# Optimization experiments

Measured on AMD Instinct MI355X. Metric: run time of the kernel, lower is better.

The kernel has to match this reference:

```python
import jax, jax.numpy as jnp
import numpy as np

DIM = 512
D_IN = 4096
N_OBJ = 2048
N_REL = 32768
STEPS = 2
N_OBJ_CLS = 151
N_REL_CLS = 51
EPS = 1e-5


def _mlp2(x, w1, b1, w2, b2):
    # Linear -> ReLU -> Linear (torch Linear: y = x W^T + b)
    return jnp.maximum(x @ w1.T + b1, 0.0) @ w2.T + b2


def _gate(a, b, w, bias):
    # Sequential(Linear(2*dim, 1), Sigmoid) on cat([a, b], 1)
    return jax.nn.sigmoid(jnp.concatenate([a, b], axis=1) @ w.T + bias)


def _gru_cell(x, h, wih, whh, bih, bhh):
    gi = x @ wih.T + bih  # [N, 3*DIM]
    gh = h @ whh.T + bhh
    ir, iz, inew = jnp.split(gi, 3, axis=1)
    hr, hz, hnew = jnp.split(gh, 3, axis=1)
    r = jax.nn.sigmoid(ir + hr)
    z = jax.nn.sigmoid(iz + hz)
    n = jnp.tanh(inew + r * hnew)
    return (1.0 - z) * n + z * h


def setup_inputs() -> dict:
    key = jax.random.key(0)
    ks = jax.random.split(key, 32)
    rn = lambda k, shape, s=0.02: jax.random.normal(k, shape, dtype=jnp.float32) * s
    z = lambda *shape: jnp.zeros(shape, dtype=jnp.float32)
    return {
        'x_obj': jax.random.normal(ks[0], (N_OBJ, D_IN), dtype=jnp.float32),
        'x_pred': jax.random.normal(ks[1], (N_REL, D_IN), dtype=jnp.float32),
        'rel_inds': jax.random.randint(ks[2], (N_REL, 2), 0, N_OBJ),
        # obj / pred embedding MLPs
        'oe_w1': rn(ks[3], (DIM, D_IN)), 'oe_b1': z(DIM),
        'oe_w2': rn(ks[4], (DIM, DIM)), 'oe_b2': z(DIM),
        'pe_w1': rn(ks[5], (DIM, D_IN)), 'pe_b1': z(DIM),
        'pe_w2': rn(ks[6], (DIM, DIM)), 'pe_b2': z(DIM),
        # gates: Linear(2*dim, 1)
        'g_sn_w': rn(ks[7], (1, 2 * DIM)), 'g_sn_b': z(1),
        'g_on_w': rn(ks[8], (1, 2 * DIM)), 'g_on_b': z(1),
        'g_se_w': rn(ks[9], (1, 2 * DIM)), 'g_se_b': z(1),
        'g_oe_w': rn(ks[10], (1, 2 * DIM)), 'g_oe_b': z(1),
        # GRU cells
        'ngru_wih': rn(ks[11], (3 * DIM, DIM)), 'ngru_whh': rn(ks[12], (3 * DIM, DIM)),
        'ngru_bih': z(3 * DIM), 'ngru_bhh': z(3 * DIM),
        'egru_wih': rn(ks[13], (3 * DIM, DIM)), 'egru_whh': rn(ks[14], (3 * DIM, DIM)),
        'egru_bih': z(3 * DIM), 'egru_bhh': z(3 * DIM),
        # classifier heads
        'op_w': rn(ks[15], (N_OBJ_CLS, DIM)), 'op_b': z(N_OBJ_CLS),
        'pp_w': rn(ks[16], (N_REL_CLS, DIM)), 'pp_b': z(N_REL_CLS),
    }


def reference(x_obj, x_pred, rel_inds,
              oe_w1, oe_b1, oe_w2, oe_b2,
              pe_w1, pe_b1, pe_w2, pe_b2,
              g_sn_w, g_sn_b, g_on_w, g_on_b,
              g_se_w, g_se_b, g_oe_w, g_oe_b,
              ngru_wih, ngru_whh, ngru_bih, ngru_bhh,
              egru_wih, egru_whh, egru_bih, egru_bhh,
              op_w, op_b, pp_w, pp_b):
    n_obj = x_obj.shape[0]
    subj_idx = rel_inds[:, 0]
    obj_idx = rel_inds[:, 1]

    h_obj = _mlp2(x_obj, oe_w1, oe_b1, oe_w2, oe_b2)    # [N_obj, DIM]
    h_edge = _mlp2(x_pred, pe_w1, pe_b1, pe_w2, pe_b2)  # [N_rel, DIM]

    # row sums of the 0/1 subj/obj_pred_map == in-degree counts (constants)
    ones = jnp.ones((rel_inds.shape[0],), dtype=jnp.float32)
    cnt_s = jax.ops.segment_sum(ones, subj_idx, num_segments=n_obj)[:, None]
    cnt_o = jax.ops.segment_sum(ones, obj_idx, num_segments=n_obj)[:, None]

    for _ in range(STEPS):
        sub_vert = h_obj[subj_idx]  # [N_rel, DIM]
        obj_vert = h_obj[obj_idx]

        # node update: gated edge->node messages, mean-aggregated per node
        msg_p2s = _gate(sub_vert, h_edge, g_sn_w, g_sn_b) * h_edge
        msg_p2o = _gate(obj_vert, h_edge, g_on_w, g_on_b) * h_edge
        node_message = (
            jax.ops.segment_sum(msg_p2s, subj_idx, num_segments=n_obj) / (cnt_s + EPS)
            + jax.ops.segment_sum(msg_p2o, obj_idx, num_segments=n_obj) / (cnt_o + EPS)
        ) / 2.0
        new_h_obj = _gru_cell(node_message, h_obj, ngru_wih, ngru_whh, ngru_bih, ngru_bhh)

        # edge update: gated node->edge messages
        msg_s2p = _gate(sub_vert, h_edge, g_se_w, g_se_b) * sub_vert
        msg_o2p = _gate(obj_vert, h_edge, g_oe_w, g_oe_b) * obj_vert
        edge_message = (msg_s2p + msg_o2p) / 2.0
        h_edge = _gru_cell(edge_message, h_edge, egru_wih, egru_whh, egru_bih, egru_bhh)
        h_obj = new_h_obj

    obj_class_logits = h_obj @ op_w.T + op_b    # [N_obj, 151]
    pred_class_logits = h_edge @ pp_w.T + pp_b  # [N_rel, 51]
    obj_class_labels = jnp.argmax(obj_class_logits[:, 1:], axis=1) + 1
    return (h_obj, h_edge, obj_class_logits, pred_class_logits, obj_class_labels, rel_inds)
```

## Files before the change

kernel.cpp:

```cpp
#include <hip/hip_runtime.h>
#include <math.h>

typedef unsigned short u16;
typedef unsigned int u32;
typedef _Float16 f16;
typedef f16 f16x8 __attribute__((ext_vector_type(8)));
typedef float f32x4 __attribute__((ext_vector_type(4)));

#define DIM 512
#define D_IN 4096
#define N_OBJS 2048
#define N_RELS 32768
#define N_OBJ_CLS 151
#define N_REL_CLS 51
#define EPSV 1e-5f

#define OFF_HOBJ  0
#define OFF_HEDGE (N_OBJS*DIM)
#define OFF_OLOG  (OFF_HEDGE + N_RELS*DIM)
#define OFF_PLOG  (OFF_OLOG + N_OBJS*N_OBJ_CLS)
#define OFF_LBL   (OFF_PLOG + N_RELS*N_REL_CLS)
#define OFF_RI    (OFF_LBL + N_OBJS)

__device__ __forceinline__ float sigmoidf_(float x) { return 1.0f / (1.0f + expf(-x)); }
__device__ __forceinline__ u16 f2h_(float f) {
    union { f16 h; u16 u; } c; c.h = (f16)f; return c.u;
}
__device__ __forceinline__ float h2f_(u16 u) {
    union { f16 h; u16 u; } c; c.u = u; return (float)c.h;
}

__device__ __forceinline__ void cvt8h1(const float* f, uint4& h) {
    u32 hh[8];
#pragma unroll
    for (int i = 0; i < 8; i++) hh[i] = f2h_(f[i]);
    h.x = hh[0] | (hh[1] << 16); h.y = hh[2] | (hh[3] << 16);
    h.z = hh[4] | (hh[5] << 16); h.w = hh[6] | (hh[7] << 16);
}
__device__ __forceinline__ void cvt8h2(const float* f, uint4& h, uint4& l) {
    u32 hh[8], ll[8];
#pragma unroll
    for (int i = 0; i < 8; i++) {
        u16 x = f2h_(f[i]);
        hh[i] = x;
        ll[i] = f2h_(f[i] - h2f_(x));
    }
    h.x = hh[0] | (hh[1] << 16); h.y = hh[2] | (hh[3] << 16);
    h.z = hh[4] | (hh[5] << 16); h.w = hh[6] | (hh[7] << 16);
    l.x = ll[0] | (ll[1] << 16); l.y = ll[2] | (ll[3] << 16);
    l.z = ll[4] | (ll[5] << 16); l.w = ll[6] | (ll[7] << 16);
}

__device__ __forceinline__ int swzo(int row, int c) {
    return row * 32 + ((c ^ ((row >> 1) & 3)) << 3);
}

__device__ __forceinline__ int xcdswz(int orig, int nwg) {
    const int q = nwg >> 3;
    return (orig & 7) * q + (orig >> 3);
}

__device__ __forceinline__ void gload16(const void* g, void* l) {
    __builtin_amdgcn_global_load_lds(
        (const __attribute__((address_space(1))) void*)g,
        (__attribute__((address_space(3))) void*)l, 16, 0, 0);
}

#define Q_BIG  (DIM * D_IN / 4)
#define Q_SQ   (DIM * DIM / 4)
#define Q_GRU  (3 * DIM * DIM / 4)
#define Q_OP   (N_OBJ_CLS * DIM / 4)
#define Q_PP   (N_REL_CLS * DIM / 4)
#define CV_C0  (Q_BIG)
#define CV_C1  (CV_C0 + Q_BIG)
#define CV_C2  (CV_C1 + Q_SQ)
#define CV_C3  (CV_C2 + Q_SQ)
#define CV_C4  (CV_C3 + Q_GRU)
#define CV_C5  (CV_C4 + Q_GRU)
#define CV_C6  (CV_C5 + Q_GRU)
#define CV_C7  (CV_C6 + Q_GRU)
#define CV_C8  (CV_C7 + Q_OP)
#define CV_C9  (CV_C8 + Q_PP)

__global__ __launch_bounds__(256) void convert_all(
    const float* __restrict__ s0, u16* __restrict__ d0,
    const float* __restrict__ s1, u16* __restrict__ d1,
    const float* __restrict__ s2, u16* __restrict__ d2,
    const float* __restrict__ s3, u16* __restrict__ d3,
    const float* __restrict__ s4, u16* __restrict__ d4,
    const float* __restrict__ s5, u16* __restrict__ d5,
    const float* __restrict__ s6, u16* __restrict__ d6,
    const float* __restrict__ s7, u16* __restrict__ d7,
    const float* __restrict__ s8, u16* __restrict__ d8,
    const float* __restrict__ s9, u16* __restrict__ d9)
{
    int i = blockIdx.x * 256 + threadIdx.x;
    if (i >= CV_C9) return;
    const float* src; u16* dst; int base;
    if      (i < CV_C0) { src = s0; dst = d0; base = 0; }
    else if (i < CV_C1) { src = s1; dst = d1; base = CV_C0; }
    else if (i < CV_C2) { src = s2; dst = d2; base = CV_C1; }
    else if (i < CV_C3) { src = s3; dst = d3; base = CV_C2; }
    else if (i < CV_C4) { src = s4; dst = d4; base = CV_C3; }
    else if (i < CV_C5) { src = s5; dst = d5; base = CV_C4; }
    else if (i < CV_C6) { src = s6; dst = d6; base = CV_C5; }
    else if (i < CV_C7) { src = s7; dst = d7; base = CV_C6; }
    else if (i < CV_C8) { src = s8; dst = d8; base = CV_C7; }
    else                { src = s9; dst = d9; base = CV_C8; }
    const int q = i - base;
    const float4 v = ((const float4*)src)[q];
    ((ushort4*)dst)[q] = make_ushort4(f2h_(v.x), f2h_(v.y), f2h_(v.z), f2h_(v.w));
}

template<bool RELU, int AT, bool WSPLIT>
__device__ __forceinline__ void gemm_a32_body(
    int id, u16* sAh, u16* sBh, u16* sAl,
    const float* __restrict__ A, const u16* __restrict__ Bhi,
    const float* __restrict__ bias, u16* __restrict__ Chi, u16* __restrict__ Clo,
    int NX, int K)
{
    const int m0 = (id / NX) * 128, n0 = (id % NX) * 128;
    const int N = NX * 128;
    const int t = threadIdx.x;
    const int wid = t >> 6, lane = t & 63;
    const int wm = (wid >> 1) * 64, wn = (wid & 1) * 64;
    const int lr = lane & 15, lk = lane >> 4;

    f32x4 acc[4][4] = {};

    const int sr = t >> 1;
    const int sc = (t & 1) * 2;
    const float* Ap = A + (size_t)(m0 + sr) * K + (t & 1) * 16;

    const int rB = (wid * 2) * 16 + (lane >> 2);
    const int cB = (lane & 3) ^ ((rB >> 1) & 3);
    const u16* Bp0 = Bhi + (size_t)(n0 + rB) * K + cB * 8;
    const u16* Bp1 = Bp0 + (size_t)16 * K;
    u16* Bd0 = &sBh[(wid * 2) * 512];
    u16* Bd1 = Bd0 + 512;

    float fv[16];
    *(float4*)&fv[0]  = *(const float4*)(Ap);
    *(float4*)&fv[4]  = *(const float4*)(Ap + 4);
    *(float4*)&fv[8]  = *(const float4*)(Ap + 8);
    *(float4*)&fv[12] = *(const float4*)(Ap + 12);

    for (int k0 = 0; k0 < K; k0 += 32) {
        uint4 ah0, ah1, al0, al1;
        if (AT == 2) { cvt8h2(fv, ah0, al0); cvt8h2(fv + 8, ah1, al1); }
        else         { cvt8h1(fv, ah0);      cvt8h1(fv + 8, ah1); }

        __syncthreads();
        gload16(Bp0 + k0, Bd0);
        gload16(Bp1 + k0, Bd1);
        *(uint4*)&sAh[swzo(sr, sc)]     = ah0;
        *(uint4*)&sAh[swzo(sr, sc + 1)] = ah1;
        if (AT == 2) {
            *(uint4*)&sAl[swzo(sr, sc)]     = al0;
            *(uint4*)&sAl[swzo(sr, sc + 1)] = al1;
        }
        asm volatile("s_waitcnt vmcnt(0)" ::: "memory");
        __syncthreads();

        const int kn = k0 + 32;
        if (kn < K) {
            *(float4*)&fv[0]  = *(const float4*)(Ap + kn);
            *(float4*)&fv[4]  = *(const float4*)(Ap + kn + 4);
            *(float4*)&fv[8]  = *(const float4*)(Ap + kn + 8);
            *(float4*)&fv[12] = *(const float4*)(Ap + kn + 12);
        }

        f16x8 ah[4], al[4], bh[4];
#pragma unroll
        for (int f = 0; f < 4; f++) {
            const int off = swzo(wm + f * 16 + lr, lk);
            ah[f] = *(const f16x8*)&sAh[off];
            if (AT == 2) al[f] = *(const f16x8*)&sAl[off];
            bh[f] = *(const f16x8*)&sBh[swzo(wn + f * 16 + lr, lk)];
        }
#pragma unroll
        for (int fm = 0; fm < 4; fm++)
#pragma unroll
            for (int fn = 0; fn < 4; fn++) {
                acc[fm][fn] = __builtin_amdgcn_mfma_f32_16x16x32_f16(ah[fm], bh[fn], acc[fm][fn], 0, 0, 0);
                if (AT == 2)
                    acc[fm][fn] = __builtin_amdgcn_mfma_f32_16x16x32_f16(al[fm], bh[fn], acc[fm][fn], 0, 0, 0);
            }
    }
#pragma unroll
    for (int fm = 0; fm < 4; fm++) {
        const int mrow = m0 + wm + fm * 16 + lk * 4;
#pragma unroll
        for (int fn = 0; fn < 4; fn++) {
            const int col = n0 + wn + fn * 16 + lr;
            const float bv = bias[col];
#pragma unroll
            for (int j = 0; j < 4; j++) {
                float v = acc[fm][fn][j] + bv;
                if (RELU) v = fmaxf(v, 0.0f);
                const u16 h = f2h_(v);
                Chi[(size_t)(mrow + j) * N + col] = h;
                if (WSPLIT) Clo[(size_t)(mrow + j) * N + col] = f2h_(v - h2f_(h));
            }
        }
    }
}

__global__ __launch_bounds__(256, 3) void enc1_both(
    const float* __restrict__ xp, const u16* __restrict__ pw,
    const float* __restrict__ pb, u16* __restrict__ tmpe,
    const float* __restrict__ xo, const u16* __restrict__ ow,
    const float* __restrict__ ob, u16* __restrict__ tmpoh, u16* __restrict__ tmpol)
{
    __shared__ u16 smem[3 * 4096];
    const int id = xcdswz(blockIdx.x, gridDim.x);
    if (id < 1024)
        gemm_a32_body<true, 1, false>(id, smem, smem + 4096, nullptr,
                                      xp, pw, pb, tmpe, nullptr, 4, D_IN);
    else
        gemm_a32_body<true, 2, true>(id - 1024, smem, smem + 4096, smem + 8192,
                                     xo, ow, ob, tmpoh, tmpol, 4, D_IN);
}

template<int AT, bool WF32, bool WHI, bool WLO>
__device__ __forceinline__ void gemm_f16_body(
    int id, u16* smem,
    const u16* __restrict__ Ahi, const u16* __restrict__ Alo,
    const u16* __restrict__ Bhi, const float* __restrict__ bias,
    float* __restrict__ C32, u16* __restrict__ Chi, u16* __restrict__ Clo,
    int NX, int N, int ldc, int K)
{
    const int m0 = (id / NX) * 128, n0 = (id % NX) * 128;
    const int t = threadIdx.x;
    const int wid = t >> 6, lane = t & 63;
    const int wm = (wid >> 1) * 64, wn = (wid & 1) * 64;
    const int lr = lane & 15, lk = lane >> 4;

    f32x4 acc[4][4] = {};

    const int rr = (wid * 2) * 16 + (lane >> 2);
    const int cc = (lane & 3) ^ ((rr >> 1) & 3);
    const u16* pA0 = Ahi + (size_t)(m0 + rr) * K + cc * 8;
    const u16* pA1 = pA0 + (size_t)16 * K;
    const u16* pL0 = (AT == 2) ? Alo + (size_t)(m0 + rr) * K + cc * 8 : nullptr;
    const u16* pL1 = (AT == 2) ? pL0 + (size_t)16 * K : nullptr;
    const u16* pB0 = Bhi + (size_t)(n0 + rr) * K + cc * 8;
    const u16* pB1 = pB0 + (size_t)16 * K;
    const int bOff = (wid * 2) * 512;

    for (int k0 = 0; k0 < K; k0 += 64) {
        __syncthreads();
#pragma unroll
        for (int h = 0; h < 2; h++) {
            const int kk = k0 + h * 32;
            u16* sA_ = smem + h * 4096;
            u16* sB_ = smem + 8192 + h * 4096;
            gload16(pA0 + kk, sA_ + bOff);
            gload16(pA1 + kk, sA_ + bOff + 512);
            if (AT == 2) {
                u16* sL_ = smem + 16384 + h * 4096;
                gload16(pL0 + kk, sL_ + bOff);
                gload16(pL1 + kk, sL_ + bOff + 512);
            }
            gload16(pB0 + kk, sB_ + bOff);
            gload16(pB1 + kk, sB_ + bOff + 512);
        }
        asm volatile("s_waitcnt vmcnt(0)" ::: "memory");
        __syncthreads();

#pragma unroll
        for (int h = 0; h < 2; h++) {
            const u16* sA_ = smem + h * 4096;
            const u16* sB_ = smem + 8192 + h * 4096;
            const u16* sL_ = smem + 16384 + h * 4096;
            f16x8 ah[4], al[4], bh[4];
#pragma unroll
            for (int f = 0; f < 4; f++) {
                const int off = swzo(wm + f * 16 + lr, lk);
                ah[f] = *(const f16x8*)&sA_[off];
                if (AT == 2) al[f] = *(const f16x8*)&sL_[off];
                bh[f] = *(const f16x8*)&sB_[swzo(wn + f * 16 + lr, lk)];
            }
#pragma unroll
            for (int fm = 0; fm < 4; fm++)
#pragma unroll
                for (int fn = 0; fn < 4; fn++) {
                    acc[fm][fn] = __builtin_amdgcn_mfma_f32_16x16x32_f16(ah[fm], bh[fn], acc[fm][fn], 0, 0, 0);
                    if (AT == 2)
                        acc[fm][fn] = __builtin_amdgcn_mfma_f32_16x16x32_f16(al[fm], bh[fn], acc[fm][fn], 0, 0, 0);
                }
        }
    }
#pragma unroll
    for (int fm = 0; fm < 4; fm++) {
        const int mrow = m0 + wm + fm * 16 + lk * 4;
#pragma unroll
        for (int fn = 0; fn < 4; fn++) {
            const int col = n0 + wn + fn * 16 + lr;
            const float bv = bias[col];
#pragma unroll
            for (int j = 0; j < 4; j++) {
                const float v = acc[fm][fn][j] + bv;
                if (WF32 && col < N) C32[(size_t)(mrow + j) * ldc + col] = v;
                if (WHI) {
                    const u16 h = f2h_(v);
                    Chi[(size_t)(mrow + j) * (NX * 128) + col] = h;
                    if (WLO)
                        Clo[(size_t)(mrow + j) * (NX * 128) + col] = f2h_(v - h2f_(h));
                }
            }
        }
    }
}

template<int AT, bool WF32, bool WHI, bool WLO>
__global__ __launch_bounds__(256, AT == 1 ? 4 : 3) void gemm_f16(
    const u16* __restrict__ Ahi, const u16* __restrict__ Alo,
    const u16* __restrict__ Bhi, const float* __restrict__ bias,
    float* __restrict__ C32, u16* __restrict__ Chi, u16* __restrict__ Clo,
    int NX, int N, int ldc, int K)
{
    __shared__ u16 smem[AT == 2 ? 6 * 4096 : 4 * 4096];
    const int id = xcdswz(blockIdx.x, gridDim.x);
    gemm_f16_body<AT, WF32, WHI, WLO>(id, smem, Ahi, Alo, Bhi, bias,
                                      C32, Chi, Clo, NX, N, ldc, K);
}

__global__ __launch_bounds__(256, 3) void cls_both(
    const u16* __restrict__ hhe, const u16* __restrict__ pph,
    const float* __restrict__ ppb, float* __restrict__ plog,
    const u16* __restrict__ hhoh, const u16* __restrict__ hhol,
    const u16* __restrict__ oph, const float* __restrict__ opb,
    float* __restrict__ olog)
{
    __shared__ u16 smem[6 * 4096];
    const int id = xcdswz(blockIdx.x, gridDim.x);
    if (id < 256)
        gemm_f16_body<1, true, false, false>(id, smem, hhe, nullptr, pph, ppb,
                                             plog, nullptr, nullptr,
                                             1, N_REL_CLS, N_REL_CLS, DIM);
    else
        gemm_f16_body<2, true, false, false>(id - 256, smem, hhoh, hhol, oph, opb,
                                             olog, nullptr, nullptr,
                                             2, N_OBJ_CLS, N_OBJ_CLS, DIM);
}

__global__ __launch_bounds__(256, 4) void gru_gemm_e(
    const u16* __restrict__ Xh, const u16* __restrict__ WiH,
    const float* __restrict__ bi, u16* __restrict__ gi,
    const u16* __restrict__ Hh, const u16* __restrict__ WhH,
    const float* __restrict__ bhs, u16* __restrict__ gh_)
{
    __shared__ u16 smem[4 * 4096];
    const int id = xcdswz(blockIdx.x, gridDim.x);
    const int part = id % 24;
    const int m0b = id / 24;
    const bool isH = part >= 12;
    const int nblk = part - (isH ? 12 : 0);
    gemm_f16_body<1, false, true, false>(m0b * 12 + nblk, smem,
        isH ? Hh : Xh, nullptr, isH ? WhH : WiH, isH ? bhs : bi,
        nullptr, isH ? gh_ : gi, nullptr, 12, 1536, 1536, DIM);
}

__global__ __launch_bounds__(256, 4) void gru_all1(
    const u16* __restrict__ Xe, const u16* __restrict__ WeI,
    const float* __restrict__ beI, u16* __restrict__ geI,
    const u16* __restrict__ He, const u16* __restrict__ WeH,
    const float* __restrict__ beH, u16* __restrict__ geH,
    int nEdge,
    const u16* __restrict__ Xoh, const u16* __restrict__ Xol,
    const u16* __restrict__ Hoh, const u16* __restrict__ Hol,
    const u16* __restrict__ WoI, const u16* __restrict__ WoH,
    const float* __restrict__ boI, const float* __restrict__ boH,
    const float* __restrict__ zb,
    u16* __restrict__ gioh, u16* __restrict__ giol,
    u16* __restrict__ ghoh, u16* __restrict__ ghol)
{
    __shared__ u16 smem[4 * 4096];
    const int id = xcdswz(blockIdx.x, gridDim.x);
    if (id < nEdge) {
        const int part = id % 24;
        const int m0b = id / 24;
        const bool isH = part >= 12;
        const int nblk = part - (isH ? 12 : 0);
        gemm_f16_body<1, false, true, false>(m0b * 12 + nblk, smem,
            isH ? He : Xe, nullptr, isH ? WeH : WeI, isH ? beH : beI,
            nullptr, isH ? geH : geI, nullptr, 12, 1536, 1536, DIM);
    } else if (id < nEdge + 384) {
        const int oid = id - nEdge;
        const int part = oid % 24;
        const int m0b = oid / 24;
        const bool isH = part >= 12;
        const int nblk = part - (isH ? 12 : 0);
        gemm_f16_body<1, false, true, false>(m0b * 12 + nblk, smem,
            isH ? Hoh : Xoh, nullptr, isH ? WoH : WoI, isH ? boH : boI,
            nullptr, isH ? ghoh : gioh, nullptr, 12, 1536, 1536, DIM);
    } else {
        const int oid = id - nEdge - 384;
        const int part = oid % 24;
        const int m0b = oid / 24;
        const bool isH = part >= 12;
        const int nblk = part - (isH ? 12 : 0);
        gemm_f16_body<1, false, true, false>(m0b * 12 + nblk, smem,
            isH ? Hol : Xol, nullptr, isH ? WoH : WoI, zb,
            nullptr, isH ? ghol : giol, nullptr, 12, 1536, 1536, DIM);
    }
}

__device__ __forceinline__ float gcomb(float ir, float iz, float in_,
                                       float hr, float hz, float hn, float h) {
    const float r = sigmoidf_(ir + hr);
    const float z = sigmoidf_(iz + hz);
    const float n = tanhf(in_ + r * hn);
    return (1.0f - z) * n + z * h;
}

template<bool WF32>
__global__ __launch_bounds__(256) void gru_combine(
    const u16* __restrict__ gi, const u16* __restrict__ gh,
    u16* __restrict__ hh, float* __restrict__ H32, int R)
{
    const int idx = blockIdx.x * 256 + threadIdx.x;
    if (idx >= R * 128) return;
    const int r = idx >> 7, c4 = (idx & 127) * 4;
    const size_t gb = (size_t)r * 1536 + c4;
    const ushort4 ir4 = *(const ushort4*)&gi[gb];
    const ushort4 iz4 = *(const ushort4*)&gi[gb + 512];
    const ushort4 in4 = *(const ushort4*)&gi[gb + 1024];
    const ushort4 hr4 = *(const ushort4*)&gh[gb];
    const ushort4 hz4 = *(const ushort4*)&gh[gb + 512];
    const ushort4 hn4 = *(const ushort4*)&gh[gb + 1024];
    const size_t hb = (size_t)r * 512 + c4;
    const ushort4 hhi = *(const ushort4*)&hh[hb];
    float4 o;
    o.x = gcomb(h2f_(ir4.x), h2f_(iz4.x), h2f_(in4.x),
                h2f_(hr4.x), h2f_(hz4.x), h2f_(hn4.x), h2f_(hhi.x));
    o.y = gcomb(h2f_(ir4.y), h2f_(iz4.y), h2f_(in4.y),
                h2f_(hr4.y), h2f_(hz4.y), h2f_(hn4.y), h2f_(hhi.y));
    o.z = gcomb(h2f_(ir4.z), h2f_(iz4.z), h2f_(in4.z),
                h2f_(hr4.z), h2f_(hz4.z), h2f_(hn4.z), h2f_(hhi.z));
    o.w = gcomb(h2f_(ir4.w), h2f_(iz4.w), h2f_(in4.w),
                h2f_(hr4.w), h2f_(hz4.w), h2f_(hn4.w), h2f_(hhi.w));
    *(ushort4*)&hh[hb] = make_ushort4(f2h_(o.x), f2h_(o.y), f2h_(o.z), f2h_(o.w));
    if (WF32) *(float4*)&H32[hb] = o;
}

template<bool WF32>
__global__ __launch_bounds__(256) void gru_combine_o2(
    const u16* __restrict__ gih, const u16* __restrict__ gil,
    const u16* __restrict__ ghh_, const u16* __restrict__ ghl_,
    u16* __restrict__ hh, u16* __restrict__ hl, float* __restrict__ H32, int R)
{
    const int idx = blockIdx.x * 256 + threadIdx.x;
    if (idx >= R * 128) return;
    const int r = idx >> 7, c4 = (idx & 127) * 4;
    const size_t gb = (size_t)r * 1536 + c4;
    ushort4 a, b;
    float ir[4], iz[4], in_[4], hr[4], hz[4], hn[4];
    a = *(const ushort4*)&gih[gb];        b = *(const ushort4*)&gil[gb];
    ir[0] = h2f_(a.x) + h2f_(b.x); ir[1] = h2f_(a.y) + h2f_(b.y);
    ir[2] = h2f_(a.z) + h2f_(b.z); ir[3] = h2f_(a.w) + h2f_(b.w);
    a = *(const ushort4*)&gih[gb + 512];  b = *(const ushort4*)&gil[gb + 512];
    iz[0] = h2f_(a.x) + h2f_(b.x); iz[1] = h2f_(a.y) + h2f_(b.y);
    iz[2] = h2f_(a.z) + h2f_(b.z); iz[3] = h2f_(a.w) + h2f_(b.w);
    a = *(const ushort4*)&gih[gb + 1024]; b = *(const ushort4*)&gil[gb + 1024];
    in_[0] = h2f_(a.x) + h2f_(b.x); in_[1] = h2f_(a.y) + h2f_(b.y);
    in_[2] = h2f_(a.z) + h2f_(b.z); in_[3] = h2f_(a.w) + h2f_(b.w);
    a = *(const ushort4*)&ghh_[gb];        b = *(const ushort4*)&ghl_[gb];
    hr[0] = h2f_(a.x) + h2f_(b.x); hr[1] = h2f_(a.y) + h2f_(b.y);
    hr[2] = h2f_(a.z) + h2f_(b.z); hr[3] = h2f_(a.w) + h2f_(b.w);
    a = *(const ushort4*)&ghh_[gb + 512];  b = *(const ushort4*)&ghl_[gb + 512];
    hz[0] = h2f_(a.x) + h2f_(b.x); hz[1] = h2f_(a.y) + h2f_(b.y);
    hz[2] = h2f_(a.z) + h2f_(b.z); hz[3] = h2f_(a.w) + h2f_(b.w);
    a = *(const ushort4*)&ghh_[gb + 1024]; b = *(const ushort4*)&ghl_[gb + 1024];
    hn[0] = h2f_(a.x) + h2f_(b.x); hn[1] = h2f_(a.y) + h2f_(b.y);
    hn[2] = h2f_(a.z) + h2f_(b.z); hn[3] = h2f_(a.w) + h2f_(b.w);

    const size_t hb = (size_t)r * 512 + c4;
    const ushort4 hhi = *(const ushort4*)&hh[hb];
    const ushort4 hlo = *(const ushort4*)&hl[hb];
    float h[4];
    h[0] = h2f_(hhi.x) + h2f_(hlo.x); h[1] = h2f_(hhi.y) + h2f_(hlo.y);
    h[2] = h2f_(hhi.z) + h2f_(hlo.z); h[3] = h2f_(hhi.w) + h2f_(hlo.w);

    float o[4];
#pragma unroll
    for (int j = 0; j < 4; j++)
        o[j] = gcomb(ir[j], iz[j], in_[j], hr[j], hz[j], hn[j], h[j]);

    const ushort4 hi4 = make_ushort4(f2h_(o[0]), f2h_(o[1]), f2h_(o[2]), f2h_(o[3]));
    *(ushort4*)&hh[hb] = hi4;
    *(ushort4*)&hl[hb] = make_ushort4(
        f2h_(o[0] - h2f_(hi4.x)), f2h_(o[1] - h2f_(hi4.y)),
        f2h_(o[2] - h2f_(hi4.z)), f2h_(o[3] - h2f_(hi4.w)));
    if (WF32) *(float4*)&H32[hb] = make_float4(o[0], o[1], o[2], o[3]);
}

__global__ __launch_bounds__(256) void count_int(const int* __restrict__ rel,
                                                 int* cs, int* co)
{
    const int e = blockIdx.x * 256 + threadIdx.x;
    atomicAdd(&cs[rel[2 * e]], 1);
    atomicAdd(&co[rel[2 * e + 1]], 1);
}

__global__ __launch_bounds__(256) void scan_off(const int* __restrict__ cs,
    const int* __restrict__ co, int* __restrict__ offs, int* __restrict__ offo)
{
    __shared__ int tmp[256];
    for (int arr = 0; arr < 2; arr++) {
        const int* c = arr ? co : cs;
        int* off = arr ? offo : offs;
        const int base = threadIdx.x * 8;
        int loc[8]; int s = 0;
#pragma unroll
        for (int j = 0; j < 8; j++) { loc[j] = c[base + j]; s += loc[j]; }
        tmp[threadIdx.x] = s;
        __syncthreads();
        for (int d = 1; d < 256; d <<= 1) {
            const int v = (threadIdx.x >= d) ? tmp[threadIdx.x - d] : 0;
            __syncthreads();
            tmp[threadIdx.x] += v;
            __syncthreads();
        }
        int p = tmp[threadIdx.x] - s;
#pragma unroll
        for (int j = 0; j < 8; j++) { off[base + j] = p; p += loc[j]; }
        __syncthreads();
    }
}

__global__ __launch_bounds__(256) void fill_csr(const int* __restrict__ rel,
    int* curS, int* curO, const int* __restrict__ offs, const int* __restrict__ offo,
    int* __restrict__ listS, int* __restrict__ listO, float* __restrict__ outri)
{
    const int e = blockIdx.x * 256 + threadIdx.x;
    const int s = rel[2 * e], o = rel[2 * e + 1];
    const int i = atomicAdd(&curS[s], 1);
    listS[offs[s] + i] = e;
    const int j = atomicAdd(&curO[o], 1);
    listO[offo[o] + j] = e;
    outri[2 * e]     = (float)s;
    outri[2 * e + 1] = (float)o;
}

__global__ __launch_bounds__(256) void gatepass(
    const u16* __restrict__ hho, const u16* __restrict__ hhe,
    const int* __restrict__ rel,
    const float* __restrict__ wsn, const float* __restrict__ bsn,
    const float* __restrict__ won, const float* __restrict__ bon,
    const float* __restrict__ wse, const float* __restrict__ bse,
    const float* __restrict__ woe, const float* __restrict__ boe,
    const int* __restrict__ cs, const int* __restrict__ co,
    u16* __restrict__ emh, float* __restrict__ af, float* __restrict__ ag)
{
    const int e = blockIdx.x * 4 + (threadIdx.x >> 6);
    const int lane = threadIdx.x & 63;
    const int s = rel[2 * e], o = rel[2 * e + 1];
    const int c = lane * 8;

    const uint4 hsu = *(const uint4*)&hho[(size_t)s * DIM + c];
    const uint4 hou = *(const uint4*)&hho[(size_t)o * DIM + c];
    const uint4 heu = *(const uint4*)&hhe[(size_t)e * DIM + c];
    float hs[8], ho[8], he[8];
    hs[0] = h2f_((u16)hsu.x); hs[1] = h2f_((u16)(hsu.x >> 16));
    hs[2] = h2f_((u16)hsu.y); hs[3] = h2f_((u16)(hsu.y >> 16));
    hs[4] = h2f_((u16)hsu.z); hs[5] = h2f_((u16)(hsu.z >> 16));
    hs[6] = h2f_((u16)hsu.w); hs[7] = h2f_((u16)(hsu.w >> 16));
    ho[0] = h2f_((u16)hou.x); ho[1] = h2f_((u16)(hou.x >> 16));
    ho[2] = h2f_((u16)hou.y); ho[3] = h2f_((u16)(hou.y >> 16));
    ho[4] = h2f_((u16)hou.z); ho[5] = h2f_((u16)(hou.z >> 16));
    ho[6] = h2f_((u16)hou.w); ho[7] = h2f_((u16)(hou.w >> 16));
    he[0] = h2f_((u16)heu.x); he[1] = h2f_((u16)(heu.x >> 16));
    he[2] = h2f_((u16)heu.y); he[3] = h2f_((u16)(heu.y >> 16));
    he[4] = h2f_((u16)heu.z); he[5] = h2f_((u16)(heu.z >> 16));
    he[6] = h2f_((u16)heu.w); he[7] = h2f_((u16)(heu.w >> 16));

    float p0 = 0.f, p1 = 0.f, p2 = 0.f, p3 = 0.f;
#pragma unroll
    for (int q = 0; q < 2; q++) {
        const float4 w0v = *(const float4*)&wsn[c + q * 4];
        const float4 w0e = *(const float4*)&wsn[DIM + c + q * 4];
        const float4 w1v = *(const float4*)&won[c + q * 4];
        const float4 w1e = *(const float4*)&won[DIM + c + q * 4];
        const float4 w2v = *(const float4*)&wse[c + q * 4];
        const float4 w2e = *(const float4*)&wse[DIM + c + q * 4];
        const float4 w3v = *(const float4*)&woe[c + q * 4];
        const float4 w3e = *(const float4*)&woe[DIM + c + q * 4];
        const float* s4 = &hs[q * 4];
        const float* o4 = &ho[q * 4];
        const float* e4 = &he[q * 4];
        p0 += s4[0]*w0v.x + s4[1]*w0v.y + s4[2]*w0v.z + s4[3]*w0v.w
            + e4[0]*w0e.x + e4[1]*w0e.y + e4[2]*w0e.z + e4[3]*w0e.w;
        p1 += o4[0]*w1v.x + o4[1]*w1v.y + o4[2]*w1v.z + o4[3]*w1v.w
            + e4[0]*w1e.x + e4[1]*w1e.y + e4[2]*w1e.z + e4[3]*w1e.w;
        p2 += s4[0]*w2v.x + s4[1]*w2v.y + s4[2]*w2v.z + s4[3]*w2v.w
            + e4[0]*w2e.x + e4[1]*w2e.y + e4[2]*w2e.z + e4[3]*w2e.w;
        p3 += o4[0]*w3v.x + o4[1]*w3v.y + o4[2]*w3v.z + o4[3]*w3v.w
            + e4[0]*w3e.x + e4[1]*w3e.y + e4[2]*w3e.z + e4[3]*w3e.w;
    }
#pragma unroll
    for (int off = 32; off; off >>= 1) {
        p0 += __shfl_xor(p0, off);
        p1 += __shfl_xor(p1, off);
        p2 += __shfl_xor(p2, off);
        p3 += __shfl_xor(p3, off);
    }
    const float gsn = sigmoidf_(p0 + bsn[0]);
    const float gon = sigmoidf_(p1 + bon[0]);
    const float gse = sigmoidf_(p2 + bse[0]);
    const float goe = sigmoidf_(p3 + boe[0]);

    if (lane == 0) {
        af[e] = 0.5f * gsn / ((float)cs[s] + EPSV);
        ag[e] = 0.5f * gon / ((float)co[o] + EPSV);
    }
    u16 em8[8];
#pragma unroll
    for (int j = 0; j < 8; j++)
        em8[j] = f2h_(0.5f * (gse * hs[j] + goe * ho[j]));
    *(uint4*)&emh[(size_t)e * DIM + c] = *(const uint4*)em8;
}

__global__ __launch_bounds__(256) void gather_nm(
    const u16* __restrict__ hhe,
    const int* __restrict__ listS, const int* __restrict__ listO,
    const int* __restrict__ offs, const int* __restrict__ offo,
    const int* __restrict__ cs, const int* __restrict__ co,
    const float* __restrict__ af, const float* __restrict__ ag,
    u16* __restrict__ nmh, u16* __restrict__ nml)
{
    const int v = blockIdx.x * 4 + (threadIdx.x >> 6);
    const int lane = threadIdx.x & 63;
    const int c = lane * 8;

    float acc[8] = {};
#pragma unroll
    for (int side = 0; side < 2; side++) {
        const int* list = side ? listO : listS;
        const int b = side ? offo[v] : offs[v];
        const int n = side ? co[v] : cs[v];
        const float* coef = side ? ag : af;
        for (int i = 0; i < n; i++) {
            const int e = list[b + i];
            const float a = coef[e];
            const uint4 x = *(const uint4*)&hhe[(size_t)e * DIM + c];
            acc[0] += a * h2f_((u16)x.x); acc[1] += a * h2f_((u16)(x.x >> 16));
            acc[2] += a * h2f_((u16)x.y); acc[3] += a * h2f_((u16)(x.y >> 16));
            acc[4] += a * h2f_((u16)x.z); acc[5] += a * h2f_((u16)(x.z >> 16));
            acc[6] += a * h2f_((u16)x.w); acc[7] += a * h2f_((u16)(x.w >> 16));
        }
    }
    u16 hi8[8], lo8[8];
#pragma unroll
    for (int j = 0; j < 8; j++) {
        hi8[j] = f2h_(acc[j]);
        lo8[j] = f2h_(acc[j] - h2f_(hi8[j]));
    }
    *(uint4*)&nmh[(size_t)v * DIM + c] = *(const uint4*)hi8;
    *(uint4*)&nml[(size_t)v * DIM + c] = *(const uint4*)lo8;
}

__global__ __launch_bounds__(256) void argmax_kernel(const float* __restrict__ logits,
                                                     float* __restrict__ out)
{
    const int row = blockIdx.x * 4 + (threadIdx.x >> 6);
    const int lane = threadIdx.x & 63;
    float bv = -1e30f; int bi = 1;
    for (int j = 1 + lane; j < N_OBJ_CLS; j += 64) {
        const float v = logits[(size_t)row * N_OBJ_CLS + j];
        if (v > bv) { bv = v; bi = j; }
    }
#pragma unroll
    for (int off = 32; off; off >>= 1) {
        const float ov = __shfl_xor(bv, off);
        const int oi = __shfl_xor(bi, off);
        if (ov > bv || (ov == bv && oi < bi)) { bv = ov; bi = oi; }
    }
    if (lane == 0) out[row] = (float)bi;
}

extern "C" void kernel_launch(void* const* d_in, const int* in_sizes, int n_in,
                              void* d_out, int out_size, void* d_ws, size_t ws_size,
                              hipStream_t stream)
{
    const float* x_obj = (const float*)d_in[0];
    const float* x_pred = (const float*)d_in[1];
    const int* rel = (const int*)d_in[2];
    const float* oe_w1 = (const float*)d_in[3];
    const float* oe_b1 = (const float*)d_in[4];
    const float* oe_w2 = (const float*)d_in[5];
    const float* oe_b2 = (const float*)d_in[6];
    const float* pe_w1 = (const float*)d_in[7];
    const float* pe_b1 = (const float*)d_in[8];
    const float* pe_w2 = (const float*)d_in[9];
    const float* pe_b2 = (const float*)d_in[10];
    const float* g_sn_w = (const float*)d_in[11];
    const float* g_sn_b = (const float*)d_in[12];
    const float* g_on_w = (const float*)d_in[13];
    const float* g_on_b = (const float*)d_in[14];
    const float* g_se_w = (const float*)d_in[15];
    const float* g_se_b = (const float*)d_in[16];
    const float* g_oe_w = (const float*)d_in[17];
    const float* g_oe_b = (const float*)d_in[18];
    const float* ngru_wih = (const float*)d_in[19];
    const float* ngru_whh = (const float*)d_in[20];
    const float* ngru_bih = (const float*)d_in[21];
    const float* ngru_bhh = (const float*)d_in[22];
    const float* egru_wih = (const float*)d_in[23];
    const float* egru_whh = (const float*)d_in[24];
    const float* egru_bih = (const float*)d_in[25];
    const float* egru_bhh = (const float*)d_in[26];
    const float* op_w = (const float*)d_in[27];
    const float* op_b = (const float*)d_in[28];
    const float* pp_w = (const float*)d_in[29];
    const float* pp_b = (const float*)d_in[30];

    float* out = (float*)d_out;

    float* h_obj = out + OFF_HOBJ;
    float* h_edge = out + OFF_HEDGE;

    char* wsp = (char*)d_ws;
    float* af = (float*)wsp; wsp += N_RELS * 4;
    float* ag = (float*)wsp; wsp += N_RELS * 4;
    float* zbias = (float*)wsp; wsp += 1536 * 4;
    int* cs = (int*)wsp;   wsp += N_OBJS * 4;
    int* co = (int*)wsp;   wsp += N_OBJS * 4;
    int* offs = (int*)wsp; wsp += N_OBJS * 4;
    int* offo = (int*)wsp; wsp += N_OBJS * 4;
    int* curS = (int*)wsp; wsp += N_OBJS * 4;
    int* curO = (int*)wsp; wsp += N_OBJS * 4;
    int* listS = (int*)wsp; wsp += N_RELS * 4;
    int* listO = (int*)wsp; wsp += N_RELS * 4;

    u16* wp = (u16*)wsp;
    const int s_big = DIM * D_IN, s_sq = DIM * DIM, s_gru = 3 * DIM * DIM;
    u16 *oe1h = wp; wp += s_big;
    u16 *pe1h = wp; wp += s_big;
    u16 *oe2h = wp; wp += s_sq;
    u16 *pe2h = wp; wp += s_sq;
    u16 *nih_h = wp; wp += s_gru;
    u16 *nhh_h = wp; wp += s_gru;
    u16 *eih_h = wp; wp += s_gru;
    u16 *ehh_h = wp; wp += s_gru;
    u16 *oph = wp; wp += 256 * DIM;
    u16 *pph = wp; wp += 128 * DIM;
    u16 *tmpo_h = wp; wp += (size_t)N_OBJS * DIM;
    u16 *tmpo_l = wp; wp += (size_t)N_OBJS * DIM;
    u16 *tmpe_h = wp; wp += (size_t)N_RELS * DIM;
    u16 *hhoh = wp; wp += (size_t)N_OBJS * DIM;
    u16 *hhol = wp; wp += (size_t)N_OBJS * DIM;
    u16 *hhe  = wp; wp += (size_t)N_RELS * DIM;
    u16 *emh  = wp; wp += (size_t)N_RELS * DIM;
    u16 *nmh  = wp; wp += (size_t)N_OBJS * DIM;
    u16 *nml  = wp; wp += (size_t)N_OBJS * DIM;
    u16 *gioh = wp; wp += (size_t)N_OBJS * 1536;
    u16 *giol = wp; wp += (size_t)N_OBJS * 1536;
    u16 *ghoh = wp; wp += (size_t)N_OBJS * 1536;
    u16 *ghol = wp; wp += (size_t)N_OBJS * 1536;

    const size_t used = (size_t)((char*)wp - (char*)d_ws);
    int R = 8192;
    if (used + (size_t)16384 * 6144 <= ws_size) R = 16384;
    u16* gi = wp;
    u16* gh = gi + (size_t)R * 1536;

    convert_all<<<(CV_C9 + 255) / 256, 256, 0, stream>>>(
        oe_w1, oe1h, pe_w1, pe1h, oe_w2, oe2h, pe_w2, pe2h,
        ngru_wih, nih_h, ngru_whh, nhh_h, egru_wih, eih_h, egru_whh, ehh_h,
        op_w, oph, pp_w, pph);

    hipMemsetAsync(cs, 0, 2 * N_OBJS * sizeof(int), stream);
    hipMemsetAsync(curS, 0, 2 * N_OBJS * sizeof(int), stream);
    hipMemsetAsync(zbias, 0, 1536 * sizeof(float), stream);
    count_int<<<N_RELS / 256, 256, 0, stream>>>(rel, cs, co);
    scan_off<<<1, 256, 0, stream>>>(cs, co, offs, offo);
    fill_csr<<<N_RELS / 256, 256, 0, stream>>>(rel, curS, curO, offs, offo,
                                               listS, listO, out + OFF_RI);

    enc1_both<<<1088, 256, 0, stream>>>(
        x_pred, pe1h, pe_b1, tmpe_h,
        x_obj, oe1h, oe_b1, tmpo_h, tmpo_l);
    gemm_f16<1, false, true, false><<<4 * (N_RELS / 128), 256, 0, stream>>>(
        tmpe_h, nullptr, pe2h, pe_b2, nullptr, hhe, nullptr, 4, DIM, DIM, DIM);
    gemm_f16<2, false, true, true><<<4 * (N_OBJS / 128), 256, 0, stream>>>(
        tmpo_h, tmpo_l, oe2h, oe_b2, nullptr, hhoh, hhol, 4, DIM, DIM, DIM);

    for (int step = 0; step < 2; step++) {
        gatepass<<<N_RELS / 4, 256, 0, stream>>>(
            hhoh, hhe, rel,
            g_sn_w, g_sn_b, g_on_w, g_on_b, g_se_w, g_se_b, g_oe_w, g_oe_b,
            cs, co, emh, af, ag);
        gather_nm<<<N_OBJS / 4, 256, 0, stream>>>(
            hhe, listS, listO, offs, offo, cs, co, af, ag, nmh, nml);

        const int Rc0 = (N_RELS < R) ? N_RELS : R;
        const int nEdge = 24 * (Rc0 / 128);
        gru_all1<<<nEdge + 768, 256, 0, stream>>>(
            emh, eih_h, egru_bih, gi, hhe, ehh_h, egru_bhh, gh, nEdge,
            nmh, nml, hhoh, hhol, nih_h, nhh_h, ngru_bih, ngru_bhh, zbias,
            gioh, giol, ghoh, ghol);

        if (step == 0)
            gru_combine_o2<false><<<(N_OBJS * 128 + 255) / 256, 256, 0, stream>>>(
                gioh, giol, ghoh, ghol, hhoh, hhol, nullptr, N_OBJS);
        else
            gru_combine_o2<true><<<(N_OBJS * 128 + 255) / 256, 256, 0, stream>>>(
                gioh, giol, ghoh, ghol, hhoh, hhol, h_obj, N_OBJS);
        if (step == 0)
            gru_combine<false><<<(Rc0 * 128 + 255) / 256, 256, 0, stream>>>(
                gi, gh, hhe, nullptr, Rc0);
        else
            gru_combine<true><<<(Rc0 * 128 + 255) / 256, 256, 0, stream>>>(
                gi, gh, hhe, h_edge, Rc0);

        for (int r0 = Rc0; r0 < N_RELS; r0 += R) {
            const int Rc = (N_RELS - r0 < R) ? (N_RELS - r0) : R;
            gru_gemm_e<<<24 * (Rc / 128), 256, 0, stream>>>(
                emh + (size_t)r0 * DIM, eih_h, egru_bih, gi,
                hhe + (size_t)r0 * DIM, ehh_h, egru_bhh, gh);
            if (step == 0)
                gru_combine<false><<<(Rc * 128 + 255) / 256, 256, 0, stream>>>(
                    gi, gh, hhe + (size_t)r0 * DIM, nullptr, Rc);
            else
                gru_combine<true><<<(Rc * 128 + 255) / 256, 256, 0, stream>>>(
                    gi, gh, hhe + (size_t)r0 * DIM, h_edge + (size_t)r0 * DIM, Rc);
        }
    }

    cls_both<<<288, 256, 0, stream>>>(
        hhe, pph, pp_b, out + OFF_PLOG,
        hhoh, hhol, oph, op_b, out + OFF_OLOG);

    argmax_kernel<<<N_OBJS / 4, 256, 0, stream>>>(out + OFF_OLOG, out + OFF_LBL);
}
```

Measured before the change: 982.3 us.

## Pre-convert encoder inputs to fp16 and use the f16 GEMM path

Adds a kernel that converts x_pred to fp16, and x_obj to an fp16 hi/lo pair, in workspace. The first encoder layer then runs through the existing f16 GEMM with a fused ReLU instead of the fp32-A GEMM that converts inputs while loading tiles. This aims to remove the per-tile fp32 load and convert overhead in the large K=4096 GEMM. The cost is an extra full pass over the 512MB fp32 inputs plus writing about 300MB of fp16 copies. The fallback to the old kernel is kept for when the workspace is too small.

```diff
diff --git a/kernel.cpp b/kernel.cpp
--- a/kernel.cpp
+++ b/kernel.cpp
@@ -112,6 +112,27 @@
     ((ushort4*)dst)[q] = make_ushort4(f2h_(v.x), f2h_(v.y), f2h_(v.z), f2h_(v.w));
 }
 
+#define QX_PRED ((size_t)N_RELS * D_IN / 4)
+#define QX_OBJ  ((size_t)N_OBJS * D_IN / 4)
+__global__ __launch_bounds__(256) void convert_x(
+    const float* __restrict__ xp, u16* __restrict__ xph,
+    const float* __restrict__ xo, u16* __restrict__ xoh, u16* __restrict__ xol)
+{
+    const size_t i = (size_t)blockIdx.x * 256 + threadIdx.x;
+    if (i < QX_PRED) {
+        const float4 v = ((const float4*)xp)[i];
+        ((ushort4*)xph)[i] = make_ushort4(f2h_(v.x), f2h_(v.y), f2h_(v.z), f2h_(v.w));
+    } else if (i < QX_PRED + QX_OBJ) {
+        const size_t q = i - QX_PRED;
+        const float4 v = ((const float4*)xo)[q];
+        u16 h0 = f2h_(v.x), h1 = f2h_(v.y), h2 = f2h_(v.z), h3 = f2h_(v.w);
+        ((ushort4*)xoh)[q] = make_ushort4(h0, h1, h2, h3);
+        ((ushort4*)xol)[q] = make_ushort4(
+            f2h_(v.x - h2f_(h0)), f2h_(v.y - h2f_(h1)),
+            f2h_(v.z - h2f_(h2)), f2h_(v.w - h2f_(h3)));
+    }
+}
+
 template<bool RELU, int AT, bool WSPLIT>
 __device__ __forceinline__ void gemm_a32_body(
     int id, u16* sAh, u16* sBh, u16* sAl,
@@ -222,7 +243,7 @@
                                      xo, ow, ob, tmpoh, tmpol, 4, D_IN);
 }
 
-template<int AT, bool WF32, bool WHI, bool WLO>
+template<int AT, bool WF32, bool WHI, bool WLO, bool RELU>
 __device__ __forceinline__ void gemm_f16_body(
     int id, u16* smem,
     const u16* __restrict__ Ahi, const u16* __restrict__ Alo,
@@ -300,7 +321,8 @@
             const float bv = bias[col];
 #pragma unroll
             for (int j = 0; j < 4; j++) {
-                const float v = acc[fm][fn][j] + bv;
+                float v = acc[fm][fn][j] + bv;
+                if (RELU) v = fmaxf(v, 0.0f);
                 if (WF32 && col < N) C32[(size_t)(mrow + j) * ldc + col] = v;
                 if (WHI) {
                     const u16 h = f2h_(v);
@@ -313,7 +335,7 @@
     }
 }
 
-template<int AT, bool WF32, bool WHI, bool WLO>
+template<int AT, bool WF32, bool WHI, bool WLO, bool RELU>
 __global__ __launch_bounds__(256, AT == 1 ? 4 : 3) void gemm_f16(
     const u16* __restrict__ Ahi, const u16* __restrict__ Alo,
     const u16* __restrict__ Bhi, const float* __restrict__ bias,
@@ -322,8 +344,8 @@
 {
     __shared__ u16 smem[AT == 2 ? 6 * 4096 : 4 * 4096];
     const int id = xcdswz(blockIdx.x, gridDim.x);
-    gemm_f16_body<AT, WF32, WHI, WLO>(id, smem, Ahi, Alo, Bhi, bias,
-                                      C32, Chi, Clo, NX, N, ldc, K);
+    gemm_f16_body<AT, WF32, WHI, WLO, RELU>(id, smem, Ahi, Alo, Bhi, bias,
+                                            C32, Chi, Clo, NX, N, ldc, K);
 }
 
 __global__ __launch_bounds__(256, 3) void cls_both(
@@ -336,13 +358,13 @@
     __shared__ u16 smem[6 * 4096];
     const int id = xcdswz(blockIdx.x, gridDim.x);
     if (id < 256)
-        gemm_f16_body<1, true, false, false>(id, smem, hhe, nullptr, pph, ppb,
-                                             plog, nullptr, nullptr,
-                                             1, N_REL_CLS, N_REL_CLS, DIM);
+        gemm_f16_body<1, true, false, false, false>(id, smem, hhe, nullptr, pph, ppb,
+                                                    plog, nullptr, nullptr,
+                                                    1, N_REL_CLS, N_REL_CLS, DIM);
     else
-        gemm_f16_body<2, true, false, false>(id - 256, smem, hhoh, hhol, oph, opb,
-                                             olog, nullptr, nullptr,
-                                             2, N_OBJ_CLS, N_OBJ_CLS, DIM);
+        gemm_f16_body<2, true, false, false, false>(id - 256, smem, hhoh, hhol, oph, opb,
+                                                    olog, nullptr, nullptr,
+                                                    2, N_OBJ_CLS, N_OBJ_CLS, DIM);
 }
 
 __global__ __launch_bounds__(256, 4) void gru_gemm_e(
@@ -357,7 +379,7 @@
     const int m0b = id / 24;
     const bool isH = part >= 12;
     const int nblk = part - (isH ? 12 : 0);
-    gemm_f16_body<1, false, true, false>(m0b * 12 + nblk, smem,
+    gemm_f16_body<1, false, true, false, false>(m0b * 12 + nblk, smem,
         isH ? Hh : Xh, nullptr, isH ? WhH : WiH, isH ? bhs : bi,
         nullptr, isH ? gh_ : gi, nullptr, 12, 1536, 1536, DIM);
 }
@@ -383,7 +405,7 @@
         const int m0b = id / 24;
         const bool isH = part >= 12;
         const int nblk = part - (isH ? 12 : 0);
-        gemm_f16_body<1, false, true, false>(m0b * 12 + nblk, smem,
+        gemm_f16_body<1, false, true, false, false>(m0b * 12 + nblk, smem,
             isH ? He : Xe, nullptr, isH ? WeH : WeI, isH ? beH : beI,
             nullptr, isH ? geH : geI, nullptr, 12, 1536, 1536, DIM);
     } else if (id < nEdge + 384) {
@@ -392,7 +414,7 @@
         const int m0b = oid / 24;
         const bool isH = part >= 12;
         const int nblk = part - (isH ? 12 : 0);
-        gemm_f16_body<1, false, true, false>(m0b * 12 + nblk, smem,
+        gemm_f16_body<1, false, true, false, false>(m0b * 12 + nblk, smem,
             isH ? Hoh : Xoh, nullptr, isH ? WoH : WoI, isH ? boH : boI,
             nullptr, isH ? ghoh : gioh, nullptr, 12, 1536, 1536, DIM);
     } else {
@@ -401,7 +423,7 @@
         const int m0b = oid / 24;
         const bool isH = part >= 12;
         const int nblk = part - (isH ? 12 : 0);
-        gemm_f16_body<1, false, true, false>(m0b * 12 + nblk, smem,
+        gemm_f16_body<1, false, true, false, false>(m0b * 12 + nblk, smem,
             isH ? Hol : Xol, nullptr, isH ? WoH : WoI, zb,
             nullptr, isH ? ghol : giol, nullptr, 12, 1536, 1536, DIM);
     }
@@ -760,11 +782,18 @@
     u16 *ghoh = wp; wp += (size_t)N_OBJS * 1536;
     u16 *ghol = wp; wp += (size_t)N_OBJS * 1536;
 
-    const size_t used = (size_t)((char*)wp - (char*)d_ws);
+    const size_t used0 = (size_t)((char*)wp - (char*)d_ws);
     int R = 8192;
-    if (used + (size_t)16384 * 6144 <= ws_size) R = 16384;
+    if (used0 + (size_t)16384 * 6144 <= ws_size) R = 16384;
     u16* gi = wp;
     u16* gh = gi + (size_t)R * 1536;
+
+    u16* xpe_h = gh + (size_t)R * 1536;
+    u16* xo_h  = xpe_h + (size_t)N_RELS * D_IN;
+    u16* xo_l  = xo_h + (size_t)N_OBJS * D_IN;
+    const size_t need_fast =
+        (size_t)((char*)(xo_l + (size_t)N_OBJS * D_IN) - (char*)d_ws);
+    const bool fastEnc1 = (ws_size >= need_fast);
 
     convert_all<<<(CV_C9 + 255) / 256, 256, 0, stream>>>(
         oe_w1, oe1h, pe_w1, pe1h, oe_w2, oe2h, pe_w2, pe2h,
@@ -779,12 +808,22 @@
     fill_csr<<<N_RELS / 256, 256, 0, stream>>>(rel, curS, curO, offs, offo,
                                                listS, listO, out + OFF_RI);
 
-    enc1_both<<<1088, 256, 0, stream>>>(
-        x_pred, pe1h, pe_b1, tmpe_h,
-        x_obj, oe1h, oe_b1, tmpo_h, tmpo_l);
-    gemm_f16<1, false, true, false><<<4 * (N_RELS / 128), 256, 0, stream>>>(
+    if (fastEnc1) {
+        const size_t qx = QX_PRED + QX_OBJ;
+        convert_x<<<(unsigned)((qx + 255) / 256), 256, 0, stream>>>(
+            x_pred, xpe_h, x_obj, xo_h, xo_l);
+        gemm_f16<1, false, true, false, true><<<4 * (N_RELS / 128), 256, 0, stream>>>(
+            xpe_h, nullptr, pe1h, pe_b1, nullptr, tmpe_h, nullptr, 4, DIM, DIM, D_IN);
+        gemm_f16<2, false, true, true, true><<<4 * (N_OBJS / 128), 256, 0, stream>>>(
+            xo_h, xo_l, oe1h, oe_b1, nullptr, tmpo_h, tmpo_l, 4, DIM, DIM, D_IN);
+    } else {
+        enc1_both<<<1088, 256, 0, stream>>>(
+            x_pred, pe1h, pe_b1, tmpe_h,
+            x_obj, oe1h, oe_b1, tmpo_h, tmpo_l);
+    }
+    gemm_f16<1, false, true, false, false><<<4 * (N_RELS / 128), 256, 0, stream>>>(
         tmpe_h, nullptr, pe2h, pe_b2, nullptr, hhe, nullptr, 4, DIM, DIM, DIM);
-    gemm_f16<2, false, true, true><<<4 * (N_OBJS / 128), 256, 0, stream>>>(
+    gemm_f16<2, false, true, true, false><<<4 * (N_OBJS / 128), 256, 0, stream>>>(
         tmpo_h, tmpo_l, oe2h, oe_b2, nullptr, hhoh, hhol, 4, DIM, DIM, DIM);
 
     for (int step = 0; step < 2; step++) {
```

New measurement: 1.082 ms. 1.1x slower.
